# Optimization experiments

Measured on AMD Instinct MI355X. Metric: run time of the kernel, lower is better.

## Reference

```python
import jax, jax.numpy as jnp
import numpy as np


def _ohem_single(score, gt, tm):
    # score, gt, tm: (h, w) float32
    hw = score.size
    flat = score.reshape(-1)
    pos_num = jnp.sum((gt > 0.5) & (tm > 0.5))          # sum(gt>0.5) - sum((gt>0.5)&(tm<=0.5))
    neg_all = jnp.sum(gt < 0.5)

    # Branch 1: pos_num == 0 -> take top half of ALL scores as negatives
    n1 = neg_all // 2
    sorted_all = -jnp.sort(-flat)                        # descending
    thr1 = sorted_all[jnp.clip(n1 - 1, 0, hw - 1)]
    mask1 = (score >= thr1).astype(jnp.float32)

    # Branch 3: select top-(min(3*pos, neg)) negative scores
    n3 = jnp.minimum(pos_num * 3, neg_all)
    neg_flat = jnp.where(gt.reshape(-1) < 0.5, flat, -jnp.inf)
    sorted_neg = -jnp.sort(-neg_flat)                    # descending, positives pushed to end
    thr3 = sorted_neg[jnp.clip(n3 - 1, 0, hw - 1)]
    mask3 = (((score >= thr3) | (gt > 0.5)) & (tm > 0.5)).astype(jnp.float32)

    # Branch 2: pos_num > 0 and n3 == 0 -> training mask itself
    return jnp.where(pos_num == 0, mask1, jnp.where(n3 == 0, tm, mask3))


def _ohem_batch(y_true_cls, y_pred_cls, training_mask):
    # (b,1,h,w) each -> (b,1,h,w)
    f = jax.vmap(_ohem_single, in_axes=(0, 0, 0))
    m = f(y_pred_cls[:, 0], y_true_cls[:, 0], training_mask[:, 0])
    return m[:, None]


def _dice(y_true, y_pred, mask):
    eps = 1e-05
    inter = jnp.sum(y_true * y_pred * mask)
    union = jnp.sum(y_true * mask) + jnp.sum(y_pred * mask) + eps
    return 1.0 - 2.0 * inter / union


def _loss(y_true_cls, y_pred_cls, y_true_geo, y_pred_geo, training_mask):
    ohem = _ohem_batch(y_true_cls, y_pred_cls, training_mask)
    cls_loss = _dice(y_true_cls, y_pred_cls, ohem) * 0.01

    d1g, d2g, d3g, d4g, thg = jnp.split(y_true_geo, 5, axis=1)
    d1p, d2p, d3p, d4p, thp = jnp.split(y_pred_geo, 5, axis=1)
    area_gt = (d1g + d3g) * (d2g + d4g)
    area_pr = (d1p + d3p) * (d2p + d4p)
    w_union = jnp.minimum(d2g, d2p) + jnp.minimum(d4g, d4p)
    h_union = jnp.minimum(d1g, d1p) + jnp.minimum(d3g, d3p)
    area_int = w_union * h_union
    area_uni = area_gt + area_pr - area_int
    L_AABB = -jnp.log((area_int + 1.0) / (area_uni + 1.0))
    L_theta = 1.0 - jnp.cos(thp - thg)
    L_g = L_AABB + 20.0 * L_theta
    return jnp.mean(L_g * y_true_cls * training_mask) + cls_loss


def setup_inputs() -> dict:
    key = jax.random.key(0)
    k1, k2, k3, k4, k5 = jax.random.split(key, 5)
    b, h, w = 16, 640, 640
    return {
        "y_true_cls": jax.random.uniform(k1, (b, 1, h, w), dtype=jnp.float32),
        "y_pred_cls": jax.random.uniform(k2, (b, 1, h, w), dtype=jnp.float32),
        "y_true_geo": jax.random.uniform(k3, (b, 5, h, w), dtype=jnp.float32),
        "y_pred_geo": jax.random.uniform(k4, (b, 5, h, w), dtype=jnp.float32),
        "training_mask": jax.random.uniform(k5, (b, 1, h, w), dtype=jnp.float32),
    }


def reference(y_true_cls, y_pred_cls, y_true_geo, y_pred_geo, training_mask):
    return _loss(y_true_cls, y_pred_cls, y_true_geo, y_pred_geo, training_mask)
```

## Files before the change

### kernel.cpp

```cpp
#include <hip/hip_runtime.h>
#include <math.h>

#define B_IMG 16
#define HW 409600
#define HW4 102400
#define HW2 204800

#define GEO_PBI 100
#define GEO_NBLK (B_IMG * GEO_PBI)

#define P_BLK 100
#define TPB 256
#define NBLK2 (B_IMG * P_BLK)
#define DICE_SLOTS (NBLK2 + B_IMG)

#define SEL_CAP 65536
#define FIX_CAP 65536

#define OFF_GEO    0
#define OFF_DICE   12800
#define OFF_CNT    51584
#define OFF_STATE  51712
#define OFF_HA     52224
#define OFF_HB     183296
#define OFF_BCNT   314368
#define OFF_FCNT   314432
#define ZERO_BYTES (314496 - OFF_CNT)
#define ZERO_U4    (ZERO_BYTES / 16)
#define OFF_SELB   314496
#define OFF_FIXB   4508800

typedef float f32x2 __attribute__((ext_vector_type(2)));

union F4 { float4 v; float f[4]; };
union F2 { float2 v; f32x2 n; float f[2]; };

__device__ __forceinline__ f32x2 ntload2(const float* p) {
    return __builtin_nontemporal_load((const f32x2*)p);
}

__device__ __forceinline__ unsigned fkey(float x) {
    unsigned b = __float_as_uint(x);
    return b ^ ((b & 0x80000000u) ? 0xFFFFFFFFu : 0x80000000u);
}
__device__ __forceinline__ float funkey(unsigned k) {
    unsigned b = (k & 0x80000000u) ? (k ^ 0x80000000u) : ~k;
    return __uint_as_float(b);
}

__device__ __forceinline__ double wredd(double v) {
#pragma unroll
    for (int off = 32; off > 0; off >>= 1) v += __shfl_down(v, off);
    return v;
}
__device__ __forceinline__ unsigned wredu(unsigned v) {
#pragma unroll
    for (int off = 32; off > 0; off >>= 1) v += __shfl_down(v, off);
    return v;
}

__device__ void radix_scan(const unsigned* h, int NB, unsigned n,
                           unsigned& bin_out, unsigned& r_out, bool& tgt) {
    const int lane = threadIdx.x;
    const int seg = NB >> 6;
    const int base = lane * seg;
    unsigned segsum = 0;
    for (int j = 0; j < seg; ++j) segsum += h[base + j];
    unsigned suf = segsum;
#pragma unroll
    for (int off = 1; off < 64; off <<= 1) {
        unsigned v = __shfl_down(suf, off);
        if (lane + off < 64) suf += v;
    }
    unsigned above = suf - segsum;
    tgt = (suf >= n) && (above < n);
    bin_out = 0; r_out = 0;
    if (tgt) {
        unsigned cum = above;
        for (int j = base + seg - 1; j >= base; --j) {
            unsigned cb = cum;
            cum += h[j];
            if (cum >= n) { bin_out = (unsigned)j; r_out = n - cb; break; }
        }
    }
}

__global__ void __launch_bounds__(256)
k_zero(uint4* __restrict__ z) {
    const int i = blockIdx.x * 256 + threadIdx.x;
    if (i < ZERO_U4) z[i] = make_uint4(0u, 0u, 0u, 0u);
}

struct Geo13 {
    F2 s, g, m, d1g, d2g, d3g, d4g, thg, d1p, d2p, d3p, d4p, thp;
};

__device__ __forceinline__ void geo_load(Geo13& r, int idx,
        const float* __restrict__ ypc, const float* __restrict__ ytc,
        const float* __restrict__ tmk, const float* __restrict__ ytg,
        const float* __restrict__ ypg, int cb, int gb) {
    r.s.v   = ((const float2*)ypc)[cb + idx];
    r.g.v   = ((const float2*)ytc)[cb + idx];
    r.m.v   = ((const float2*)tmk)[cb + idx];
    r.d1g.n = ntload2(ytg + 2 * (gb + 0 * HW2 + idx));
    r.d2g.n = ntload2(ytg + 2 * (gb + 1 * HW2 + idx));
    r.d3g.n = ntload2(ytg + 2 * (gb + 2 * HW2 + idx));
    r.d4g.n = ntload2(ytg + 2 * (gb + 3 * HW2 + idx));
    r.thg.n = ntload2(ytg + 2 * (gb + 4 * HW2 + idx));
    r.d1p.n = ntload2(ypg + 2 * (gb + 0 * HW2 + idx));
    r.d2p.n = ntload2(ypg + 2 * (gb + 1 * HW2 + idx));
    r.d3p.n = ntload2(ypg + 2 * (gb + 2 * HW2 + idx));
    r.d4p.n = ntload2(ypg + 2 * (gb + 3 * HW2 + idx));
    r.thp.n = ntload2(ypg + 2 * (gb + 4 * HW2 + idx));
}

__device__ __forceinline__ void geo_compute(const Geo13& r, float& geo_f,
                                            unsigned& pos, unsigned& neg,
                                            unsigned long long* h) {
#pragma unroll
    for (int j = 0; j < 2; ++j) {
        const float gv = r.g.f[j], mv = r.m.f[j];
        pos += (gv > 0.5f && mv > 0.5f) ? 1u : 0u;
        const bool isneg = (gv < 0.5f);
        neg += isneg ? 1u : 0u;
        const unsigned bin = fkey(r.s.f[j]) >> 21;
        atomicAdd(&h[bin], 1ull + ((unsigned long long)(isneg ? 1u : 0u) << 32));
        const float ag = (r.d1g.f[j] + r.d3g.f[j]) * (r.d2g.f[j] + r.d4g.f[j]);
        const float ap = (r.d1p.f[j] + r.d3p.f[j]) * (r.d2p.f[j] + r.d4p.f[j]);
        const float wu = fminf(r.d2g.f[j], r.d2p.f[j]) + fminf(r.d4g.f[j], r.d4p.f[j]);
        const float hu = fminf(r.d1g.f[j], r.d1p.f[j]) + fminf(r.d3g.f[j], r.d3p.f[j]);
        const float ai = wu * hu;
        const float au = ag + ap - ai;
        const float la = __logf(__fdividef(au + 1.0f, ai + 1.0f));
        const float lt = 1.0f - __cosf(r.thp.f[j] - r.thg.f[j]);
        geo_f += (la + 20.0f * lt) * gv * mv;
    }
}

__global__ void __launch_bounds__(256)
k_geo(const float* __restrict__ ypc, const float* __restrict__ ytc,
      const float* __restrict__ ytg, const float* __restrict__ ypg,
      const float* __restrict__ tmk,
      unsigned* __restrict__ counts, unsigned* __restrict__ histA,
      unsigned* __restrict__ histB, double* __restrict__ geo_part) {
    __shared__ unsigned long long lh[2048];
    const int tid = threadIdx.x;
    const int img = blockIdx.x / GEO_PBI, blkin = blockIdx.x % GEO_PBI;
    const int cb = img * HW2;
    const int gb = img * 5 * HW2;
    const int base = blkin * 2048 + tid;

    for (int j = tid; j < 2048; j += 256) lh[j] = 0ull;
    __syncthreads();

    float geo_f = 0.0f;
    unsigned pos = 0, neg = 0;

    Geo13 A, B;
    geo_load(A, base + 0 * 256, ypc, ytc, tmk, ytg, ypg, cb, gb);
    geo_load(B, base + 1 * 256, ypc, ytc, tmk, ytg, ypg, cb, gb);
    __builtin_amdgcn_sched_barrier(0);
    geo_compute(A, geo_f, pos, neg, lh);
    geo_load(A, base + 2 * 256, ypc, ytc, tmk, ytg, ypg, cb, gb);
    __builtin_amdgcn_sched_barrier(0);
    geo_compute(B, geo_f, pos, neg, lh);
    geo_load(B, base + 3 * 256, ypc, ytc, tmk, ytg, ypg, cb, gb);
    __builtin_amdgcn_sched_barrier(0);
    geo_compute(A, geo_f, pos, neg, lh);
    geo_load(A, base + 4 * 256, ypc, ytc, tmk, ytg, ypg, cb, gb);
    __builtin_amdgcn_sched_barrier(0);
    geo_compute(B, geo_f, pos, neg, lh);
    geo_load(B, base + 5 * 256, ypc, ytc, tmk, ytg, ypg, cb, gb);
    __builtin_amdgcn_sched_barrier(0);
    geo_compute(A, geo_f, pos, neg, lh);
    geo_load(A, base + 6 * 256, ypc, ytc, tmk, ytg, ypg, cb, gb);
    __builtin_amdgcn_sched_barrier(0);
    geo_compute(B, geo_f, pos, neg, lh);
    geo_load(B, base + 7 * 256, ypc, ytc, tmk, ytg, ypg, cb, gb);
    __builtin_amdgcn_sched_barrier(0);
    geo_compute(A, geo_f, pos, neg, lh);
    geo_compute(B, geo_f, pos, neg, lh);

    const double gw = wredd((double)geo_f);
    const unsigned pw = wredu(pos), nw = wredu(neg);
    __shared__ double gred[4];
    __shared__ unsigned pr[4], nr[4];
    const int lane = tid & 63, w = tid >> 6;
    if (lane == 0) { gred[w] = gw; pr[w] = pw; nr[w] = nw; }
    __syncthreads();
    if (tid == 0) {
        geo_part[blockIdx.x] = gred[0] + gred[1] + gred[2] + gred[3];
        atomicAdd(&counts[img * 2 + 0], pr[0] + pr[1] + pr[2] + pr[3]);
        atomicAdd(&counts[img * 2 + 1], nr[0] + nr[1] + nr[2] + nr[3]);
    }
    for (int j = tid; j < 2048; j += 256) {
        const unsigned long long v = lh[j];
        const unsigned a = (unsigned)(v & 0xFFFFFFFFull);
        const unsigned b = (unsigned)(v >> 32);
        if (a) atomicAdd(&histA[img * 2048 + j], a);
        if (b) atomicAdd(&histB[img * 2048 + j], b);
    }
}

__global__ void k_scan1(const unsigned* __restrict__ counts,
                        const unsigned* __restrict__ histA,
                        const unsigned* __restrict__ histB,
                        unsigned* __restrict__ state) {
    const int img = blockIdx.x, lane = threadIdx.x;
    const unsigned pos = counts[img * 2 + 0], neg = counts[img * 2 + 1];
    unsigned branch, n = 1;
    if (pos == 0) {
        branch = 0;
        n = neg / 2; if (n < 1) n = 1;
    } else {
        const unsigned n3 = min(pos * 3u, neg);
        if (n3 == 0) branch = 1;
        else { branch = 2; n = n3; }
    }
    if (lane == 0) state[img * 8 + 0] = branch;
    if (branch == 1) return;
    __shared__ unsigned h[2048];
    const unsigned* g = (branch == 0 ? histA : histB) + img * 2048;
    for (int j = lane; j < 2048; j += 64) h[j] = g[j];
    __syncthreads();
    unsigned bin, r; bool tgt;
    radix_scan(h, 2048, n, bin, r, tgt);
    if (tgt) { state[img * 8 + 1] = bin; state[img * 8 + 2] = r; }
}

__global__ void __launch_bounds__(TPB)
k_collect2(const float* __restrict__ ypc, const float* __restrict__ ytc,
           const float* __restrict__ tmk, const unsigned* __restrict__ state,
           unsigned* __restrict__ bcnt, unsigned* __restrict__ bucket,
           unsigned* __restrict__ fcnt, float2* __restrict__ fixb,
           double* __restrict__ dice_part) {
    const int img = blockIdx.x / P_BLK, blk = blockIdx.x % P_BLK;
    const unsigned branch = state[img * 8 + 0];
    const unsigned bin = state[img * 8 + 1];
    const int cbase = img * HW4 + blk * 1024;
    const int lane = threadIdx.x & 63;
    const unsigned long long lmlt = (1ull << lane) - 1ull;
    const float4* sc = (const float4*)ypc;
    const float4* gt = (const float4*)ytc;
    const float4* tm = (const float4*)tmk;
    unsigned* bk = bucket + (size_t)img * SEL_CAP;
    float2*   fb = fixb + (size_t)img * FIX_CAP;

    float di = 0.0f, dg = 0.0f, dp = 0.0f;
#pragma unroll
    for (int k = 0; k < 4; ++k) {
        const int t = threadIdx.x + k * TPB;
        F4 s, g, m; s.v = sc[cbase + t]; g.v = gt[cbase + t]; m.v = tm[cbase + t];
        if (branch == 1) {
#pragma unroll
            for (int j = 0; j < 4; ++j) {
                const float sv = s.f[j], gv = g.f[j], mv = m.f[j];
                di += gv * sv * mv; dg += gv * mv; dp += sv * mv;
            }
        } else {
#pragma unroll
            for (int j = 0; j < 4; ++j) {
                const float sv = s.f[j], gv = g.f[j], mv = m.f[j];
                const unsigned key = fkey(sv);
                const unsigned kb = key >> 21;
                const bool cand = (branch == 0) || (gv < 0.5f);
                const bool selp = cand && (kb == bin);
                const unsigned long long msk = __ballot(selp);
                if (msk) {
                    const int leader = __ffsll((long long)msk) - 1;
                    unsigned b0 = 0;
                    if (lane == leader)
                        b0 = atomicAdd(&bcnt[img], (unsigned)__popcll(msk));
                    b0 = (unsigned)__shfl((int)b0, leader);
                    const unsigned idx = b0 + (unsigned)__popcll(msk & lmlt);
                    if (selp && idx < SEL_CAP) bk[idx] = key;
                }
                bool unc; float mm;
                if (branch == 0) {
                    unc = (kb == bin);
                    mm = (kb > bin) ? 1.0f : 0.0f;
                } else {
                    if (gv > 0.5f)       { unc = false; mm = (mv > 0.5f) ? 1.0f : 0.0f; }
                    else if (mv <= 0.5f) { unc = false; mm = 0.0f; }
                    else                 { unc = (kb == bin); mm = (kb > bin) ? 1.0f : 0.0f; }
                }
                if (!unc) { di += gv * sv * mm; dg += gv * mm; dp += sv * mm; }
                const unsigned long long msk2 = __ballot(unc);
                if (msk2) {
                    const int leader = __ffsll((long long)msk2) - 1;
                    unsigned b0 = 0;
                    if (lane == leader)
                        b0 = atomicAdd(&fcnt[img], (unsigned)__popcll(msk2));
                    b0 = (unsigned)__shfl((int)b0, leader);
                    const unsigned idx = b0 + (unsigned)__popcll(msk2 & lmlt);
                    if (unc && idx < FIX_CAP) fb[idx] = make_float2(sv, gv);
                }
            }
        }
    }
    const double a = wredd((double)di), b = wredd((double)dg), c = wredd((double)dp);
    __shared__ double r[4][3];
    const int wid = threadIdx.x >> 6;
    if (lane == 0) { r[wid][0] = a; r[wid][1] = b; r[wid][2] = c; }
    __syncthreads();
    if (threadIdx.x == 0) {
        dice_part[blockIdx.x * 3 + 0] = r[0][0] + r[1][0] + r[2][0] + r[3][0];
        dice_part[blockIdx.x * 3 + 1] = r[0][1] + r[1][1] + r[2][1] + r[3][1];
        dice_part[blockIdx.x * 3 + 2] = r[0][2] + r[1][2] + r[2][2] + r[3][2];
    }
}

__global__ void k_select(unsigned* __restrict__ state,
                         const unsigned* __restrict__ bcnt,
                         const unsigned* __restrict__ bucket) {
    const int img = blockIdx.x, lane = threadIdx.x;
    const unsigned branch = state[img * 8 + 0];
    if (branch == 1) return;
    const unsigned bin = state[img * 8 + 1];
    const unsigned r = state[img * 8 + 2];
    const unsigned cnt = min(bcnt[img], (unsigned)SEL_CAP);
    const unsigned* bk = bucket + (size_t)img * SEL_CAP;
    __shared__ unsigned h[2048];
    __shared__ unsigned sh_mid, sh_r2;
    for (int j = lane; j < 2048; j += 64) h[j] = 0;
    __syncthreads();
    for (unsigned i = lane; i < cnt; i += 64)
        atomicAdd(&h[(bk[i] >> 10) & 2047u], 1u);
    __syncthreads();
    unsigned mid, r2; bool tgt;
    radix_scan(h, 2048, r, mid, r2, tgt);
    if (tgt) { sh_mid = mid; sh_r2 = r2; }
    __syncthreads();
    mid = sh_mid; r2 = sh_r2;
    for (int j = lane; j < 1024; j += 64) h[j] = 0;
    __syncthreads();
    for (unsigned i = lane; i < cnt; i += 64) {
        const unsigned k = bk[i];
        if (((k >> 10) & 2047u) == mid) atomicAdd(&h[k & 1023u], 1u);
    }
    __syncthreads();
    unsigned low, r3;
    radix_scan(h, 1024, r2, low, r3, tgt);
    if (tgt)
        state[img * 8 + 4] = __float_as_uint(funkey((bin << 21) | (mid << 10) | low));
}

__global__ void __launch_bounds__(256)
k_fix(const unsigned* __restrict__ state, const unsigned* __restrict__ fcnt,
      const float2* __restrict__ fixb, double* __restrict__ dice_part) {
    const int img = blockIdx.x;
    const unsigned branch = state[img * 8 + 0];
    const float thr = __uint_as_float(state[img * 8 + 4]);
    double di = 0.0, dg = 0.0, dp = 0.0;
    if (branch != 1) {
        const unsigned cnt = min(fcnt[img], (unsigned)FIX_CAP);
        const float2* fb = fixb + (size_t)img * FIX_CAP;
        for (unsigned i = threadIdx.x; i < cnt; i += 256) {
            const float sv = fb[i].x, gv = fb[i].y;
            if (sv >= thr) { di += (double)(gv * sv); dg += (double)gv; dp += (double)sv; }
        }
    }
    const double a = wredd(di), b = wredd(dg), c = wredd(dp);
    __shared__ double r[4][3];
    const int lane = threadIdx.x & 63, wid = threadIdx.x >> 6;
    if (lane == 0) { r[wid][0] = a; r[wid][1] = b; r[wid][2] = c; }
    __syncthreads();
    if (threadIdx.x == 0) {
        const int slot = NBLK2 + img;
        dice_part[slot * 3 + 0] = r[0][0] + r[1][0] + r[2][0] + r[3][0];
        dice_part[slot * 3 + 1] = r[0][1] + r[1][1] + r[2][1] + r[3][1];
        dice_part[slot * 3 + 2] = r[0][2] + r[1][2] + r[2][2] + r[3][2];
    }
}

__global__ void __launch_bounds__(256)
k_out(const double* __restrict__ geo_part, const double* __restrict__ dice_part,
      float* __restrict__ out) {
    double geo = 0.0, di = 0.0, dg = 0.0, dp = 0.0;
    for (int i = threadIdx.x; i < DICE_SLOTS; i += 256) {
        if (i < GEO_NBLK) geo += geo_part[i];
        di += dice_part[i * 3 + 0];
        dg += dice_part[i * 3 + 1];
        dp += dice_part[i * 3 + 2];
    }
    geo = wredd(geo); di = wredd(di); dg = wredd(dg); dp = wredd(dp);
    __shared__ double r[4][4];
    const int lane = threadIdx.x & 63, wid = threadIdx.x >> 6;
    if (lane == 0) { r[wid][0] = geo; r[wid][1] = di; r[wid][2] = dg; r[wid][3] = dp; }
    __syncthreads();
    if (threadIdx.x == 0) {
        geo = r[0][0] + r[1][0] + r[2][0] + r[3][0];
        di  = r[0][1] + r[1][1] + r[2][1] + r[3][1];
        dg  = r[0][2] + r[1][2] + r[2][2] + r[3][2];
        dp  = r[0][3] + r[1][3] + r[2][3] + r[3][3];
        const double mean = geo / (double)((double)B_IMG * (double)HW);
        const double uni = dg + dp + 1e-05;
        const double loss = mean + 0.01 * (1.0 - 2.0 * di / uni);
        out[0] = (float)loss;
    }
}

extern "C" void kernel_launch(void* const* d_in, const int* in_sizes, int n_in,
                              void* d_out, int out_size, void* d_ws, size_t ws_size,
                              hipStream_t stream) {
    const float* ytc = (const float*)d_in[0];
    const float* ypc = (const float*)d_in[1];
    const float* ytg = (const float*)d_in[2];
    const float* ypg = (const float*)d_in[3];
    const float* tmk = (const float*)d_in[4];

    char* ws = (char*)d_ws;
    double*   geo_part  = (double*)(ws + OFF_GEO);
    double*   dice_part = (double*)(ws + OFF_DICE);
    unsigned* counts    = (unsigned*)(ws + OFF_CNT);
    unsigned* state     = (unsigned*)(ws + OFF_STATE);
    unsigned* histA     = (unsigned*)(ws + OFF_HA);
    unsigned* histB     = (unsigned*)(ws + OFF_HB);
    unsigned* bcnt      = (unsigned*)(ws + OFF_BCNT);
    unsigned* fcnt      = (unsigned*)(ws + OFF_FCNT);
    unsigned* bucket    = (unsigned*)(ws + OFF_SELB);
    float2*   fixb      = (float2*)(ws + OFF_FIXB);

    k_zero<<<(ZERO_U4 + 255) / 256, 256, 0, stream>>>((uint4*)(ws + OFF_CNT));
    k_geo<<<GEO_NBLK, 256, 0, stream>>>(ypc, ytc, ytg, ypg, tmk,
                                        counts, histA, histB, geo_part);
    k_scan1<<<B_IMG, 64, 0, stream>>>(counts, histA, histB, state);
    k_collect2<<<NBLK2, TPB, 0, stream>>>(ypc, ytc, tmk, state,
                                          bcnt, bucket, fcnt, fixb, dice_part);
    k_select<<<B_IMG, 64, 0, stream>>>(state, bcnt, bucket);
    k_fix<<<B_IMG, 256, 0, stream>>>(state, fcnt, fixb, dice_part);
    k_out<<<1, 256, 0, stream>>>(geo_part, dice_part, (float*)d_out);
}
```

Before: 105.3 us.

## Split fused geo+histogram kernel into separate class-histogram and geometry kernels

The single pass that computed the geometry loss and the per-image score histogram is split. A new k_cls kernel reads only score, gt and mask with float4 loads to build the histogram and counts. k_geo10 runs after the selection kernels, using twice as many blocks with half the work each, and rereads gt and mask alongside the geo channels. The intent is to shorten the critical path to the histogram scan and drop shared-memory atomics from the bandwidth-heavy geo kernel. In exchange, gt and mask are read twice and there is one more launch.

```diff
diff --git a/kernel.cpp b/kernel.cpp
--- a/kernel.cpp
+++ b/kernel.cpp
@@ -6,7 +6,7 @@
 #define HW4 102400
 #define HW2 204800
 
-#define GEO_PBI 100
+#define GEO_PBI 200
 #define GEO_NBLK (B_IMG * GEO_PBI)
 
 #define P_BLK 100
@@ -18,17 +18,17 @@
 #define FIX_CAP 65536
 
 #define OFF_GEO    0
-#define OFF_DICE   12800
-#define OFF_CNT    51584
-#define OFF_STATE  51712
-#define OFF_HA     52224
-#define OFF_HB     183296
-#define OFF_BCNT   314368
-#define OFF_FCNT   314432
-#define ZERO_BYTES (314496 - OFF_CNT)
+#define OFF_DICE   25600
+#define OFF_CNT    64384
+#define OFF_STATE  64512
+#define OFF_HA     65024
+#define OFF_HB     196096
+#define OFF_BCNT   327168
+#define OFF_FCNT   327232
+#define ZERO_BYTES (327296 - OFF_CNT)
 #define ZERO_U4    (ZERO_BYTES / 16)
-#define OFF_SELB   314496
-#define OFF_FIXB   4508800
+#define OFF_SELB   327296
+#define OFF_FIXB   4521600
 
 typedef float f32x2 __attribute__((ext_vector_type(2)));
 
@@ -91,17 +91,59 @@
     if (i < ZERO_U4) z[i] = make_uint4(0u, 0u, 0u, 0u);
 }
 
-struct Geo13 {
-    F2 s, g, m, d1g, d2g, d3g, d4g, thg, d1p, d2p, d3p, d4p, thp;
+__global__ void __launch_bounds__(TPB)
+k_cls(const float* __restrict__ ypc, const float* __restrict__ ytc,
+      const float* __restrict__ tmk,
+      unsigned* __restrict__ counts, unsigned* __restrict__ histA,
+      unsigned* __restrict__ histB) {
+    __shared__ unsigned long long lh[2048];
+    const int tid = threadIdx.x;
+    const int img = blockIdx.x / P_BLK, blk = blockIdx.x % P_BLK;
+    const int cbase = img * HW4 + blk * 1024;
+    for (int j = tid; j < 2048; j += TPB) lh[j] = 0ull;
+    __syncthreads();
+    const float4* sc = (const float4*)ypc;
+    const float4* gt = (const float4*)ytc;
+    const float4* tm = (const float4*)tmk;
+    unsigned pos = 0, neg = 0;
+#pragma unroll
+    for (int k = 0; k < 4; ++k) {
+        const int t = tid + k * TPB;
+        F4 s, g, m; s.v = sc[cbase + t]; g.v = gt[cbase + t]; m.v = tm[cbase + t];
+#pragma unroll
+        for (int j = 0; j < 4; ++j) {
+            const float gv = g.f[j], mv = m.f[j];
+            pos += (gv > 0.5f && mv > 0.5f) ? 1u : 0u;
+            const bool isneg = (gv < 0.5f);
+            neg += isneg ? 1u : 0u;
+            const unsigned bin = fkey(s.f[j]) >> 21;
+            atomicAdd(&lh[bin], 1ull + ((unsigned long long)(isneg ? 1u : 0u) << 32));
+        }
+    }
+    const unsigned pw = wredu(pos), nw = wredu(neg);
+    __shared__ unsigned pr[4], nr[4];
+    const int lane = tid & 63, w = tid >> 6;
+    if (lane == 0) { pr[w] = pw; nr[w] = nw; }
+    __syncthreads();
+    if (tid == 0) {
+        atomicAdd(&counts[img * 2 + 0], pr[0] + pr[1] + pr[2] + pr[3]);
+        atomicAdd(&counts[img * 2 + 1], nr[0] + nr[1] + nr[2] + nr[3]);
+    }
+    for (int j = tid; j < 2048; j += TPB) {
+        const unsigned long long v = lh[j];
+        const unsigned a = (unsigned)(v & 0xFFFFFFFFull);
+        const unsigned b = (unsigned)(v >> 32);
+        if (a) atomicAdd(&histA[img * 2048 + j], a);
+        if (b) atomicAdd(&histB[img * 2048 + j], b);
+    }
+}
+
+struct Geo10 {
+    F2 d1g, d2g, d3g, d4g, thg, d1p, d2p, d3p, d4p, thp;
 };
 
-__device__ __forceinline__ void geo_load(Geo13& r, int idx,
-        const float* __restrict__ ypc, const float* __restrict__ ytc,
-        const float* __restrict__ tmk, const float* __restrict__ ytg,
-        const float* __restrict__ ypg, int cb, int gb) {
-    r.s.v   = ((const float2*)ypc)[cb + idx];
-    r.g.v   = ((const float2*)ytc)[cb + idx];
-    r.m.v   = ((const float2*)tmk)[cb + idx];
+__device__ __forceinline__ void geo_load(Geo10& r, int idx,
+        const float* __restrict__ ytg, const float* __restrict__ ypg, int gb) {
     r.d1g.n = ntload2(ytg + 2 * (gb + 0 * HW2 + idx));
     r.d2g.n = ntload2(ytg + 2 * (gb + 1 * HW2 + idx));
     r.d3g.n = ntload2(ytg + 2 * (gb + 2 * HW2 + idx));
@@ -114,17 +156,11 @@
     r.thp.n = ntload2(ypg + 2 * (gb + 4 * HW2 + idx));
 }
 
-__device__ __forceinline__ void geo_compute(const Geo13& r, float& geo_f,
-                                            unsigned& pos, unsigned& neg,
-                                            unsigned long long* h) {
+__device__ __forceinline__ void geo_compute(const Geo10& r, const F2& g, const F2& m,
+                                            float& geo_f) {
 #pragma unroll
     for (int j = 0; j < 2; ++j) {
-        const float gv = r.g.f[j], mv = r.m.f[j];
-        pos += (gv > 0.5f && mv > 0.5f) ? 1u : 0u;
-        const bool isneg = (gv < 0.5f);
-        neg += isneg ? 1u : 0u;
-        const unsigned bin = fkey(r.s.f[j]) >> 21;
-        atomicAdd(&h[bin], 1ull + ((unsigned long long)(isneg ? 1u : 0u) << 32));
+        const float gv = g.f[j], mv = m.f[j];
         const float ag = (r.d1g.f[j] + r.d3g.f[j]) * (r.d2g.f[j] + r.d4g.f[j]);
         const float ap = (r.d1p.f[j] + r.d3p.f[j]) * (r.d2p.f[j] + r.d4p.f[j]);
         const float wu = fminf(r.d2g.f[j], r.d2p.f[j]) + fminf(r.d4g.f[j], r.d4p.f[j]);
@@ -137,69 +173,46 @@
     }
 }
 
-__global__ void __launch_bounds__(256)
-k_geo(const float* __restrict__ ypc, const float* __restrict__ ytc,
-      const float* __restrict__ ytg, const float* __restrict__ ypg,
-      const float* __restrict__ tmk,
-      unsigned* __restrict__ counts, unsigned* __restrict__ histA,
-      unsigned* __restrict__ histB, double* __restrict__ geo_part) {
-    __shared__ unsigned long long lh[2048];
+__global__ void k_geo10(const float* __restrict__ ytc, const float* __restrict__ tmk,
+                        const float* __restrict__ ytg, const float* __restrict__ ypg,
+                        double* __restrict__ geo_part) {
     const int tid = threadIdx.x;
     const int img = blockIdx.x / GEO_PBI, blkin = blockIdx.x % GEO_PBI;
     const int cb = img * HW2;
     const int gb = img * 5 * HW2;
-    const int base = blkin * 2048 + tid;
-
-    for (int j = tid; j < 2048; j += 256) lh[j] = 0ull;
-    __syncthreads();
+    const int base = blkin * 1024 + tid;
 
     float geo_f = 0.0f;
-    unsigned pos = 0, neg = 0;
-
-    Geo13 A, B;
-    geo_load(A, base + 0 * 256, ypc, ytc, tmk, ytg, ypg, cb, gb);
-    geo_load(B, base + 1 * 256, ypc, ytc, tmk, ytg, ypg, cb, gb);
+    Geo10 A, B;
+    F2 gA, mA, gB, mB, gA2, mA2, gB2, mB2;
+
+    geo_load(A, base + 0 * 256, ytg, ypg, gb);
+    gA.v = ((const float2*)ytc)[cb + base + 0 * 256];
+    mA.v = ((const float2*)tmk)[cb + base + 0 * 256];
+    geo_load(B, base + 1 * 256, ytg, ypg, gb);
+    gB.v = ((const float2*)ytc)[cb + base + 1 * 256];
+    mB.v = ((const float2*)tmk)[cb + base + 1 * 256];
     __builtin_amdgcn_sched_barrier(0);
-    geo_compute(A, geo_f, pos, neg, lh);
-    geo_load(A, base + 2 * 256, ypc, ytc, tmk, ytg, ypg, cb, gb);
+    geo_compute(A, gA, mA, geo_f);
+    geo_load(A, base + 2 * 256, ytg, ypg, gb);
+    gA2.v = ((const float2*)ytc)[cb + base + 2 * 256];
+    mA2.v = ((const float2*)tmk)[cb + base + 2 * 256];
     __builtin_amdgcn_sched_barrier(0);
-    geo_compute(B, geo_f, pos, neg, lh);
-    geo_load(B, base + 3 * 256, ypc, ytc, tmk, ytg, ypg, cb, gb);
+    geo_compute(B, gB, mB, geo_f);
+    geo_load(B, base + 3 * 256, ytg, ypg, gb);
+    gB2.v = ((const float2*)ytc)[cb + base + 3 * 256];
+    mB2.v = ((const float2*)tmk)[cb + base + 3 * 256];
     __builtin_amdgcn_sched_barrier(0);
-    geo_compute(A, geo_f, pos, neg, lh);
-    geo_load(A, base + 4 * 256, ypc, ytc, tmk, ytg, ypg, cb, gb);
-    __builtin_amdgcn_sched_barrier(0);
-    geo_compute(B, geo_f, pos, neg, lh);
-    geo_load(B, base + 5 * 256, ypc, ytc, tmk, ytg, ypg, cb, gb);
-    __builtin_amdgcn_sched_barrier(0);
-    geo_compute(A, geo_f, pos, neg, lh);
-    geo_load(A, base + 6 * 256, ypc, ytc, tmk, ytg, ypg, cb, gb);
-    __builtin_amdgcn_sched_barrier(0);
-    geo_compute(B, geo_f, pos, neg, lh);
-    geo_load(B, base + 7 * 256, ypc, ytc, tmk, ytg, ypg, cb, gb);
-    __builtin_amdgcn_sched_barrier(0);
-    geo_compute(A, geo_f, pos, neg, lh);
-    geo_compute(B, geo_f, pos, neg, lh);
+    geo_compute(A, gA2, mA2, geo_f);
+    geo_compute(B, gB2, mB2, geo_f);
 
     const double gw = wredd((double)geo_f);
-    const unsigned pw = wredu(pos), nw = wredu(neg);
     __shared__ double gred[4];
-    __shared__ unsigned pr[4], nr[4];
     const int lane = tid & 63, w = tid >> 6;
-    if (lane == 0) { gred[w] = gw; pr[w] = pw; nr[w] = nw; }
-    __syncthreads();
-    if (tid == 0) {
+    if (lane == 0) gred[w] = gw;
+    __syncthreads();
+    if (tid == 0)
         geo_part[blockIdx.x] = gred[0] + gred[1] + gred[2] + gred[3];
-        atomicAdd(&counts[img * 2 + 0], pr[0] + pr[1] + pr[2] + pr[3]);
-        atomicAdd(&counts[img * 2 + 1], nr[0] + nr[1] + nr[2] + nr[3]);
-    }
-    for (int j = tid; j < 2048; j += 256) {
-        const unsigned long long v = lh[j];
-        const unsigned a = (unsigned)(v & 0xFFFFFFFFull);
-        const unsigned b = (unsigned)(v >> 32);
-        if (a) atomicAdd(&histA[img * 2048 + j], a);
-        if (b) atomicAdd(&histB[img * 2048 + j], b);
-    }
 }
 
 __global__ void k_scan1(const unsigned* __restrict__ counts,
@@ -377,11 +390,13 @@
 k_out(const double* __restrict__ geo_part, const double* __restrict__ dice_part,
       float* __restrict__ out) {
     double geo = 0.0, di = 0.0, dg = 0.0, dp = 0.0;
-    for (int i = threadIdx.x; i < DICE_SLOTS; i += 256) {
-        if (i < GEO_NBLK) geo += geo_part[i];
-        di += dice_part[i * 3 + 0];
-        dg += dice_part[i * 3 + 1];
-        dp += dice_part[i * 3 + 2];
+    for (int i = threadIdx.x; i < GEO_NBLK; i += 256) {
+        geo += geo_part[i];
+        if (i < DICE_SLOTS) {
+            di += dice_part[i * 3 + 0];
+            dg += dice_part[i * 3 + 1];
+            dp += dice_part[i * 3 + 2];
+        }
     }
     geo = wredd(geo); di = wredd(di); dg = wredd(dg); dp = wredd(dp);
     __shared__ double r[4][4];
@@ -422,12 +437,12 @@
     float2*   fixb      = (float2*)(ws + OFF_FIXB);
 
     k_zero<<<(ZERO_U4 + 255) / 256, 256, 0, stream>>>((uint4*)(ws + OFF_CNT));
-    k_geo<<<GEO_NBLK, 256, 0, stream>>>(ypc, ytc, ytg, ypg, tmk,
-                                        counts, histA, histB, geo_part);
+    k_cls<<<NBLK2, TPB, 0, stream>>>(ypc, ytc, tmk, counts, histA, histB);
     k_scan1<<<B_IMG, 64, 0, stream>>>(counts, histA, histB, state);
     k_collect2<<<NBLK2, TPB, 0, stream>>>(ypc, ytc, tmk, state,
                                           bcnt, bucket, fcnt, fixb, dice_part);
     k_select<<<B_IMG, 64, 0, stream>>>(state, bcnt, bucket);
     k_fix<<<B_IMG, 256, 0, stream>>>(state, fcnt, fixb, dice_part);
+    k_geo10<<<GEO_NBLK, 256, 0, stream>>>(ytc, tmk, ytg, ypg, geo_part);
     k_out<<<1, 256, 0, stream>>>(geo_part, dice_part, (float*)d_out);
 }
```

Result: slower. 123.5 us (+17.3%).
